# Kernel tuning notes

Hardware: AMD Instinct MI355X
Metric: run time of the kernel (lower is better)

Reference implementation:

```python
import jax, jax.numpy as jnp
import numpy as np

WH, WW = 7, 7
N = WH * WW
NUM_HEADS = 12
DIM = 384
NUM_WINDOWS = 64
B = 64

def _relative_position_index(wh, ww):
    ch, cw = np.meshgrid(np.arange(wh), np.arange(ww), indexing='ij')
    coords = np.stack([ch, cw]).reshape(2, -1)            # [2, N]
    rel = coords[:, :, None] - coords[:, None, :]         # [2, N, N]
    rel = rel.transpose(1, 2, 0).astype(np.int64)         # [N, N, 2]
    rel[:, :, 0] += wh - 1
    rel[:, :, 1] += ww - 1
    rel[:, :, 0] *= 2 * ww - 1
    return rel.sum(-1)                                    # [N, N]

REL_IDX = jnp.asarray(_relative_position_index(WH, WW))  # [N, N] int

def setup_inputs() -> dict:
    key = jax.random.key(0)
    ks = jax.random.split(key, 4)
    s = 0.02
    return {
        'x': jax.random.normal(ks[0], (NUM_WINDOWS * B, N, DIM), jnp.float32),
        'mask': jnp.zeros((NUM_WINDOWS, N, N), jnp.float32),
        'w_qkv': jax.random.normal(ks[1], (3 * DIM, DIM), jnp.float32) * s,
        'b_qkv': jnp.zeros((3 * DIM,), jnp.float32),
        'w_proj': jax.random.normal(ks[2], (DIM, DIM), jnp.float32) * s,
        'b_proj': jnp.zeros((DIM,), jnp.float32),
        'bias_table': jax.random.normal(ks[3], (169, NUM_HEADS), jnp.float32) * s,
    }

def reference(x, mask, w_qkv, b_qkv, w_proj, b_proj, bias_table):
    bn, n, dim = x.shape
    h = NUM_HEADS
    d = dim // h
    scale = d ** -0.5
    # qkv projection: [bn, n, 3*dim] -> q,k,v each [bn, h, n, d]
    qkv = x @ w_qkv.T + b_qkv
    qkv = qkv.reshape(bn, n, 3, h, d).transpose(2, 0, 3, 1, 4)
    q, k, v = qkv[0], qkv[1], qkv[2]
    # windowed QK^T
    scores = jnp.einsum('bhid,bhjd->bhij', q, k) * scale
    # gathered relative position bias: [N, N, h] -> [h, N, N]
    rel_bias = bias_table[REL_IDX]                       # [N, N, h]
    scores = scores + rel_bias.transpose(2, 0, 1)[None]  # [bn, h, N, N]
    # additive window mask; batch layout is (num_windows, B)
    num_w = mask.shape[0]
    scores = scores.reshape(num_w, bn // num_w, h, n, n) + mask[:, None, None, :, :]
    scores = scores.reshape(bn, h, n, n)
    probs = jax.nn.softmax(scores, axis=-1)
    ctx = jnp.einsum('bhij,bhjd->bhid', probs, v)
    ctx = ctx.transpose(0, 2, 1, 3).reshape(bn, n, dim)  # b i (h d)
    return ctx @ w_proj.T + b_proj
```

## Files before the change

### kernel.cpp

```cpp
#include <hip/hip_runtime.h>
#include <hip/hip_fp16.h>

#define NTOK   49
#define DIMM   384
#define NHEAD  12
#define HD     32
#define BNWIN  4096

typedef _Float16 half8 __attribute__((ext_vector_type(8)));
typedef float    f32x4 __attribute__((ext_vector_type(4)));

#define WQF_OFF   0u
#define WPF_OFF   884736u
#define RBM_OFF   1179648u
#define XHF_OFF   8555520u

__global__ __launch_bounds__(256) void prep_kernel(
    const float* __restrict__ wqkv, const float* __restrict__ wproj,
    const float* __restrict__ btab, const float* __restrict__ mask,
    _Float16* __restrict__ wqf, _Float16* __restrict__ wpf,
    float* __restrict__ rbm)
{
    int idx = blockIdx.x * 256 + threadIdx.x;
    if (idx < 55296) {
        int lane = idx & 63;
        int kk   = (idx >> 6) % 12;
        int T    = idx / 768;
        const float* s = wqkv + (size_t)(T * 16 + (lane & 15)) * DIMM + kk * 32 + (lane >> 4) * 8;
        _Float16* d = wqf + (size_t)idx * 8;
#pragma unroll
        for (int e = 0; e < 8; ++e) d[e] = (_Float16)s[e];
    }
    if (idx < 18432) {
        int lane = idx & 63;
        int kk   = (idx >> 6) % 12;
        int T    = idx / 768;
        const float* s = wproj + (size_t)(T * 16 + (lane & 15)) * DIMM + kk * 32 + (lane >> 4) * 8;
        _Float16* d = wpf + (size_t)idx * 8;
#pragma unroll
        for (int e = 0; e < 8; ++e) d[e] = (_Float16)s[e];
    }
    if (idx < 1843968) {
        int wm  = idx / 28812;
        int rem = idx - wm * 28812;
        int h   = rem / 2401;
        int ij  = rem - h * 2401;
        int i   = ij / 49;
        int j   = ij - i * 49;
        int ih = i / 7, iw = i - ih * 7;
        int jh = j / 7, jw = j - jh * 7;
        int rel = (ih - jh + 6) * 13 + (iw - jw + 6);
        rbm[idx] = btab[rel * 12 + h] + mask[wm * 2401 + ij];
    }
}

__global__ __launch_bounds__(256) void xswz_kernel(
    const float* __restrict__ x, _Float16* __restrict__ xh)
{
    const int total = BNWIN * 12 * NTOK * 4;
    int g = blockIdx.x * 256 + threadIdx.x;
    const int step = gridDim.x * 256;
    for (; g < total; g += step) {
        int quad = g & 3;
        int t    = g >> 2;
        int row  = t % 49;
        int t2   = t / 49;
        int k    = t2 % 12;
        int bn   = t2 / 12;
        const float* s = x + ((size_t)bn * NTOK + row) * DIMM + k * 32 + quad * 8;
        float4 a0 = *(const float4*)s;
        float4 a1 = *(const float4*)(s + 4);
        half8 v;
        v[0] = (_Float16)a0.x; v[1] = (_Float16)a0.y;
        v[2] = (_Float16)a0.z; v[3] = (_Float16)a0.w;
        v[4] = (_Float16)a1.x; v[5] = (_Float16)a1.y;
        v[6] = (_Float16)a1.z; v[7] = (_Float16)a1.w;
        *(half8*)(xh + (size_t)g * 8) = v;
    }
}

__global__ __launch_bounds__(256, 3) void attn_kernel(
    const _Float16* __restrict__ xh,
    const _Float16* __restrict__ wq, const float* __restrict__ bq,
    const float* __restrict__ rbm,
    const _Float16* __restrict__ wp, const float* __restrict__ bp,
    float* __restrict__ out)
{
    __shared__ _Float16 smem[4][6224];
    const int tid  = threadIdx.x;
    const int wv   = tid >> 6;
    const int lane = tid & 63;
    const int quad = lane >> 4;
    const int l16  = lane & 15;
    const int bn   = blockIdx.x;
    const int wm   = bn >> 6;

    _Float16* q_s  = &smem[wv][0];
    _Float16* k_s  = &smem[wv][1960];
    _Float16* p_s  = &smem[wv][0];
    _Float16* vT_s = &smem[wv][3920];
    _Float16* cl   = &smem[0][0];

    const float scale = 0.17677669529663687f;

    int rowm[4];
#pragma unroll
    for (int mi = 0; mi < 4; ++mi) {
        int r = mi * 16 + l16;
        rowm[mi] = r > 48 ? 48 : r;
    }

    auto load_af = [&](int k, half8* af) {
        const _Float16* base = xh + ((size_t)(bn * 12 + k) * NTOK) * 32 + quad * 8;
#pragma unroll
        for (int mi = 0; mi < 4; ++mi)
            af[mi] = *(const half8*)(base + rowm[mi] * 32);
    };
    auto load_bf = [&](const _Float16* w, int T, int k) -> half8 {
        return *(const half8*)(w + ((size_t)(T * 12 + k) * 64 + lane) * 8);
    };

    half8 oh[2][4];
    f32x4 o2[4][2];

    for (int hh = 0; hh < 3; ++hh) {
        const int h = wv + (hh << 2);

        {
            f32x4 av[2][4];
#pragma unroll
            for (int nv = 0; nv < 2; ++nv)
#pragma unroll
                for (int mi = 0; mi < 4; ++mi)
                    av[nv][mi] = (f32x4){0.f, 0.f, 0.f, 0.f};

#pragma unroll 4
            for (int k = 0; k < 12; ++k) {
                half8 af[4];
                load_af(k, af);
#pragma unroll
                for (int nv = 0; nv < 2; ++nv) {
                    const int T = 48 + h * 2 + nv;
                    half8 bf = load_bf(wq, T, k);
#pragma unroll
                    for (int mi = 0; mi < 4; ++mi)
                        av[nv][mi] = __builtin_amdgcn_mfma_f32_16x16x32_f16(af[mi], bf, av[nv][mi], 0, 0, 0);
                }
            }
#pragma unroll
            for (int nv = 0; nv < 2; ++nv) {
                const float bias = bq[(48 + h * 2 + nv) * 16 + l16];
                const int colh = nv * 16 + l16;
#pragma unroll
                for (int mi = 0; mi < 4; ++mi)
#pragma unroll
                    for (int r = 0; r < 4; ++r) {
                        const int row = mi * 16 + quad * 4 + r;
                        vT_s[colh * 72 + row] = (_Float16)(av[nv][mi][r] + bias);
                    }
            }
        }

        {
            f32x4 aqk[4][4];
#pragma unroll
            for (int nn = 0; nn < 4; ++nn)
#pragma unroll
                for (int mi = 0; mi < 4; ++mi)
                    aqk[nn][mi] = (f32x4){0.f, 0.f, 0.f, 0.f};

#pragma unroll 2
            for (int k = 0; k < 12; ++k) {
                half8 af[4];
                load_af(k, af);
#pragma unroll
                for (int nn = 0; nn < 4; ++nn) {
                    const int T = (nn < 2) ? (h * 2 + nn) : (24 + h * 2 + (nn - 2));
                    half8 bf = load_bf(wq, T, k);
#pragma unroll
                    for (int mi = 0; mi < 4; ++mi)
                        aqk[nn][mi] = __builtin_amdgcn_mfma_f32_16x16x32_f16(af[mi], bf, aqk[nn][mi], 0, 0, 0);
                }
            }
#pragma unroll
            for (int nn = 0; nn < 4; ++nn) {
                const int T = (nn < 2) ? (h * 2 + nn) : (24 + h * 2 + (nn - 2));
                const float bias = bq[T * 16 + l16];
                const int colh = (nn & 1) * 16 + l16;
                if (nn < 2) {
                    const float bs = bias * scale;
#pragma unroll
                    for (int mi = 0; mi < 4; ++mi)
#pragma unroll
                        for (int r = 0; r < 4; ++r) {
                            const int row = mi * 16 + quad * 4 + r;
                            if (row < 49) q_s[row * 40 + colh] = (_Float16)(aqk[nn][mi][r] * scale + bs);
                        }
                } else {
#pragma unroll
                    for (int mi = 0; mi < 4; ++mi)
#pragma unroll
                        for (int r = 0; r < 4; ++r) {
                            const int row = mi * 16 + quad * 4 + r;
                            if (row < 49) k_s[row * 40 + colh] = (_Float16)(aqk[nn][mi][r] + bias);
                        }
                }
            }
        }

        f32x4 s[4][4];
        {
            half8 bk[4];
#pragma unroll
            for (int nj = 0; nj < 4; ++nj)
                bk[nj] = *(const half8*)(k_s + rowm[nj] * 40 + quad * 8);
#pragma unroll
            for (int mi = 0; mi < 4; ++mi) {
                half8 aq = *(const half8*)(q_s + rowm[mi] * 40 + quad * 8);
#pragma unroll
                for (int nj = 0; nj < 4; ++nj)
                    s[mi][nj] = __builtin_amdgcn_mfma_f32_16x16x32_f16(
                        aq, bk[nj], (f32x4){0.f, 0.f, 0.f, 0.f}, 0, 0, 0);
            }
        }

        const float* rbmh = rbm + (size_t)(wm * 12 + h) * 2401;
#pragma unroll
        for (int mi = 0; mi < 4; ++mi) {
#pragma unroll
            for (int r = 0; r < 4; ++r) {
                const int i  = mi * 16 + quad * 4 + r;
                const int iq = i > 48 ? 48 : i;
                float vals[4];
                float mx = -3.0e38f;
#pragma unroll
                for (int nj = 0; nj < 4; ++nj) {
                    const int j = nj * 16 + l16;
                    float v = -1.0e30f;
                    if (j < 49)
                        v = s[mi][nj][r] + rbmh[iq * 49 + j];
                    vals[nj] = v;
                    mx = fmaxf(mx, v);
                }
#pragma unroll
                for (int off = 8; off >= 1; off >>= 1)
                    mx = fmaxf(mx, __shfl_xor(mx, off));
                float sum = 0.f;
#pragma unroll
                for (int nj = 0; nj < 4; ++nj) {
                    vals[nj] = __expf(vals[nj] - mx);
                    sum += vals[nj];
                }
#pragma unroll
                for (int off = 8; off >= 1; off >>= 1)
                    sum += __shfl_xor(sum, off);
                const float inv = __builtin_amdgcn_rcpf(sum);
                if (i < 49) {
#pragma unroll
                    for (int nj = 0; nj < 4; ++nj)
                        p_s[i * 72 + nj * 16 + l16] = (_Float16)(vals[nj] * inv);
                }
            }
        }

        f32x4 o[4][2];
#pragma unroll
        for (int mi = 0; mi < 4; ++mi)
#pragma unroll
            for (int nd = 0; nd < 2; ++nd)
                o[mi][nd] = (f32x4){0.f, 0.f, 0.f, 0.f};
#pragma unroll
        for (int ks = 0; ks < 2; ++ks) {
            half8 bv[2];
#pragma unroll
            for (int nd = 0; nd < 2; ++nd)
                bv[nd] = *(const half8*)(vT_s + (nd * 16 + l16) * 72 + ks * 32 + quad * 8);
#pragma unroll
            for (int mi = 0; mi < 4; ++mi) {
                half8 apf = *(const half8*)(p_s + rowm[mi] * 72 + ks * 32 + quad * 8);
#pragma unroll
                for (int nd = 0; nd < 2; ++nd)
                    o[mi][nd] = __builtin_amdgcn_mfma_f32_16x16x32_f16(apf, bv[nd], o[mi][nd], 0, 0, 0);
            }
        }

        if (hh < 2) {
#pragma unroll
            for (int mi = 0; mi < 4; ++mi) {
                half8 t;
#pragma unroll
                for (int nd = 0; nd < 2; ++nd)
#pragma unroll
                    for (int r = 0; r < 4; ++r)
                        t[nd * 4 + r] = (_Float16)o[mi][nd][r];
                oh[hh][mi] = t;
            }
        } else {
#pragma unroll
            for (int mi = 0; mi < 4; ++mi)
#pragma unroll
                for (int nd = 0; nd < 2; ++nd)
                    o2[mi][nd] = o[mi][nd];
        }
    }

    __syncthreads();
#pragma unroll
    for (int hh = 0; hh < 2; ++hh) {
        const int h = wv + (hh << 2);
#pragma unroll
        for (int mi = 0; mi < 4; ++mi)
#pragma unroll
            for (int nd = 0; nd < 2; ++nd)
#pragma unroll
                for (int r = 0; r < 4; ++r) {
                    const int row = mi * 16 + quad * 4 + r;
                    if (row < 49)
                        cl[row * 400 + h * HD + nd * 16 + l16] = oh[hh][mi][nd * 4 + r];
                }
    }
    {
        const int h = wv + 8;
#pragma unroll
        for (int mi = 0; mi < 4; ++mi)
#pragma unroll
            for (int nd = 0; nd < 2; ++nd)
#pragma unroll
                for (int r = 0; r < 4; ++r) {
                    const int row = mi * 16 + quad * 4 + r;
                    if (row < 49)
                        cl[row * 400 + h * HD + nd * 16 + l16] = (_Float16)o2[mi][nd][r];
                }
    }
    __syncthreads();

    {
        f32x4 c[6][4];
#pragma unroll
        for (int nj = 0; nj < 6; ++nj)
#pragma unroll
            for (int mi = 0; mi < 4; ++mi)
                c[nj][mi] = (f32x4){0.f, 0.f, 0.f, 0.f};

#pragma unroll 2
        for (int k = 0; k < 12; ++k) {
            half8 a[4];
#pragma unroll
            for (int mi = 0; mi < 4; ++mi)
                a[mi] = *(const half8*)(cl + rowm[mi] * 400 + k * 32 + quad * 8);
#pragma unroll
            for (int nj = 0; nj < 6; ++nj) {
                half8 b = load_bf(wp, wv * 6 + nj, k);
#pragma unroll
                for (int mi = 0; mi < 4; ++mi)
                    c[nj][mi] = __builtin_amdgcn_mfma_f32_16x16x32_f16(a[mi], b, c[nj][mi], 0, 0, 0);
            }
        }
#pragma unroll
        for (int nj = 0; nj < 6; ++nj) {
            const int n = (wv * 6 + nj) * 16 + l16;
            const float bias = bp[n];
#pragma unroll
            for (int mi = 0; mi < 4; ++mi) {
#pragma unroll
                for (int r = 0; r < 4; ++r) {
                    const int i = mi * 16 + quad * 4 + r;
                    if (i < 49)
                        out[((size_t)bn * NTOK + i) * DIMM + n] = c[nj][mi][r] + bias;
                }
            }
        }
    }
}

extern "C" void kernel_launch(void* const* d_in, const int* in_sizes, int n_in,
                              void* d_out, int out_size, void* d_ws, size_t ws_size,
                              hipStream_t stream)
{
    const float* x     = (const float*)d_in[0];
    const float* mask  = (const float*)d_in[1];
    const float* wqkv  = (const float*)d_in[2];
    const float* bqkv  = (const float*)d_in[3];
    const float* wproj = (const float*)d_in[4];
    const float* bproj = (const float*)d_in[5];
    const float* btab  = (const float*)d_in[6];
    float* out = (float*)d_out;

    char* ws = (char*)d_ws;
    _Float16* wq_f = (_Float16*)(ws + WQF_OFF);
    _Float16* wp_f = (_Float16*)(ws + WPF_OFF);
    float*    rbm  = (float*)(ws + RBM_OFF);
    _Float16* xh_f = (_Float16*)(ws + XHF_OFF);

    hipLaunchKernelGGL(prep_kernel, dim3(7203), dim3(256), 0, stream,
                       wqkv, wproj, btab, mask, wq_f, wp_f, rbm);
    hipLaunchKernelGGL(xswz_kernel, dim3(2048), dim3(256), 0, stream, x, xh_f);
    hipLaunchKernelGGL(attn_kernel, dim3(BNWIN), dim3(256), 0, stream,
                       xh_f, wq_f, bqkv, rbm, wp_f, bproj, out);
}
```

Measured before the change: 1.543 ms.

## Fuse QKV projections, pre-swizzle fp16 bias-mask, stage output stores through LDS

Q, K and V projections are merged into a single k-loop with six accumulator tiles, so each x fragment is loaded once per head instead of twice. The relative-bias-plus-mask table is precomputed in fp16, laid out to match the MFMA fragment layout, and padded with a large negative value, so each lane does vector loads without bounds checks. Blocks are remapped so consecutive blocks hit different mask windows. The output tile is staged through LDS for coalesced float4 global stores, and the LDS row stride is padded to cut bank conflicts. The costs are higher register pressure from 24 accumulators and extra barriers around the two store passes.

Result: faster. 1.440 ms (-6.7%).

```diff
diff --git a/kernel.cpp b/kernel.cpp
--- a/kernel.cpp
+++ b/kernel.cpp
@@ -8,18 +8,19 @@
 #define BNWIN  4096
 
 typedef _Float16 half8 __attribute__((ext_vector_type(8)));
+typedef _Float16 half4 __attribute__((ext_vector_type(4)));
 typedef float    f32x4 __attribute__((ext_vector_type(4)));
 
 #define WQF_OFF   0u
 #define WPF_OFF   884736u
-#define RBM_OFF   1179648u
-#define XHF_OFF   8555520u
+#define RBMF_OFF  1179648u
+#define XHF_OFF   7471104u
 
 __global__ __launch_bounds__(256) void prep_kernel(
     const float* __restrict__ wqkv, const float* __restrict__ wproj,
     const float* __restrict__ btab, const float* __restrict__ mask,
     _Float16* __restrict__ wqf, _Float16* __restrict__ wpf,
-    float* __restrict__ rbm)
+    _Float16* __restrict__ rbmf)
 {
     int idx = blockIdx.x * 256 + threadIdx.x;
     if (idx < 55296) {
@@ -40,17 +41,28 @@
 #pragma unroll
         for (int e = 0; e < 8; ++e) d[e] = (_Float16)s[e];
     }
-    if (idx < 1843968) {
-        int wm  = idx / 28812;
-        int rem = idx - wm * 28812;
-        int h   = rem / 2401;
-        int ij  = rem - h * 2401;
-        int i   = ij / 49;
-        int j   = ij - i * 49;
-        int ih = i / 7, iw = i - ih * 7;
-        int jh = j / 7, jw = j - jh * 7;
-        int rel = (ih - jh + 6) * 13 + (iw - jw + 6);
-        rbm[idx] = btab[rel * 12 + h] + mask[wm * 2401 + ij];
+    if (idx < 3145728) {
+        int wm  = idx >> 15;
+        wm = idx / 49152;
+        int rem = idx - wm * 49152;
+        int h   = rem / 4096;
+        int e   = rem - h * 4096;
+        int r    = e & 3;
+        int lane = (e >> 2) & 63;
+        int t    = e >> 8;
+        int nj   = t & 3;
+        int mi   = t >> 2;
+        int i = mi * 16 + (lane >> 4) * 4 + r;
+        int j = nj * 16 + (lane & 15);
+        float val = -30000.f;
+        if (j < 49) {
+            int ii = i > 48 ? 48 : i;
+            int ih = ii / 7, iw = ii - ih * 7;
+            int jh = j / 7,  jw = j - jh * 7;
+            int rel = (ih - jh + 6) * 13 + (iw - jw + 6);
+            val = btab[rel * 12 + h] + mask[wm * 2401 + ii * 49 + j];
+        }
+        rbmf[idx] = (_Float16)val;
     }
 }
 
@@ -82,7 +94,7 @@
 __global__ __launch_bounds__(256, 3) void attn_kernel(
     const _Float16* __restrict__ xh,
     const _Float16* __restrict__ wq, const float* __restrict__ bq,
-    const float* __restrict__ rbm,
+    const _Float16* __restrict__ rbmf,
     const _Float16* __restrict__ wp, const float* __restrict__ bp,
     float* __restrict__ out)
 {
@@ -92,7 +104,7 @@
     const int lane = tid & 63;
     const int quad = lane >> 4;
     const int l16  = lane & 15;
-    const int bn   = blockIdx.x;
+    const int bn   = ((blockIdx.x & 7) << 9) | (blockIdx.x >> 3);
     const int wm   = bn >> 6;
 
     _Float16* q_s  = &smem[wv][0];
@@ -100,6 +112,7 @@
     _Float16* p_s  = &smem[wv][0];
     _Float16* vT_s = &smem[wv][3920];
     _Float16* cl   = &smem[0][0];
+    float*    fls  = (float*)&smem[0][0];
 
     const float scale = 0.17677669529663687f;
 
@@ -125,86 +138,60 @@
 
     for (int hh = 0; hh < 3; ++hh) {
         const int h = wv + (hh << 2);
-
-        {
-            f32x4 av[2][4];
-#pragma unroll
-            for (int nv = 0; nv < 2; ++nv)
+        int tT[6];
+        tT[0] = h * 2;      tT[1] = h * 2 + 1;
+        tT[2] = 24 + h * 2; tT[3] = 25 + h * 2;
+        tT[4] = 48 + h * 2; tT[5] = 49 + h * 2;
+
+        f32x4 acc[6][4];
+#pragma unroll
+        for (int t = 0; t < 6; ++t)
+#pragma unroll
+            for (int mi = 0; mi < 4; ++mi)
+                acc[t][mi] = (f32x4){0.f, 0.f, 0.f, 0.f};
+
+#pragma unroll 2
+        for (int k = 0; k < 12; ++k) {
+            half8 af[4];
+            load_af(k, af);
+#pragma unroll
+            for (int t = 0; t < 6; ++t) {
+                half8 bf = load_bf(wq, tT[t], k);
 #pragma unroll
                 for (int mi = 0; mi < 4; ++mi)
-                    av[nv][mi] = (f32x4){0.f, 0.f, 0.f, 0.f};
-
-#pragma unroll 4
-            for (int k = 0; k < 12; ++k) {
-                half8 af[4];
-                load_af(k, af);
-#pragma unroll
-                for (int nv = 0; nv < 2; ++nv) {
-                    const int T = 48 + h * 2 + nv;
-                    half8 bf = load_bf(wq, T, k);
-#pragma unroll
-                    for (int mi = 0; mi < 4; ++mi)
-                        av[nv][mi] = __builtin_amdgcn_mfma_f32_16x16x32_f16(af[mi], bf, av[nv][mi], 0, 0, 0);
-                }
-            }
-#pragma unroll
-            for (int nv = 0; nv < 2; ++nv) {
-                const float bias = bq[(48 + h * 2 + nv) * 16 + l16];
-                const int colh = nv * 16 + l16;
+                    acc[t][mi] = __builtin_amdgcn_mfma_f32_16x16x32_f16(af[mi], bf, acc[t][mi], 0, 0, 0);
+            }
+        }
+
+#pragma unroll
+        for (int t = 0; t < 6; ++t) {
+            const float bias = bq[tT[t] * 16 + l16];
+            const int colh = (t & 1) * 16 + l16;
+            if (t < 2) {
+                const float bs = bias * scale;
 #pragma unroll
                 for (int mi = 0; mi < 4; ++mi)
 #pragma unroll
                     for (int r = 0; r < 4; ++r) {
                         const int row = mi * 16 + quad * 4 + r;
-                        vT_s[colh * 72 + row] = (_Float16)(av[nv][mi][r] + bias);
+                        if (row < 49) q_s[row * 40 + colh] = (_Float16)(acc[t][mi][r] * scale + bs);
                     }
-            }
-        }
-
-        {
-            f32x4 aqk[4][4];
-#pragma unroll
-            for (int nn = 0; nn < 4; ++nn)
+            } else if (t < 4) {
 #pragma unroll
                 for (int mi = 0; mi < 4; ++mi)
-                    aqk[nn][mi] = (f32x4){0.f, 0.f, 0.f, 0.f};
-
-#pragma unroll 2
-            for (int k = 0; k < 12; ++k) {
-                half8 af[4];
-                load_af(k, af);
-#pragma unroll
-                for (int nn = 0; nn < 4; ++nn) {
-                    const int T = (nn < 2) ? (h * 2 + nn) : (24 + h * 2 + (nn - 2));
-                    half8 bf = load_bf(wq, T, k);
-#pragma unroll
-                    for (int mi = 0; mi < 4; ++mi)
-                        aqk[nn][mi] = __builtin_amdgcn_mfma_f32_16x16x32_f16(af[mi], bf, aqk[nn][mi], 0, 0, 0);
-                }
-            }
-#pragma unroll
-            for (int nn = 0; nn < 4; ++nn) {
-                const int T = (nn < 2) ? (h * 2 + nn) : (24 + h * 2 + (nn - 2));
-                const float bias = bq[T * 16 + l16];
-                const int colh = (nn & 1) * 16 + l16;
-                if (nn < 2) {
-                    const float bs = bias * scale;
-#pragma unroll
-                    for (int mi = 0; mi < 4; ++mi)
-#pragma unroll
-                        for (int r = 0; r < 4; ++r) {
-                            const int row = mi * 16 + quad * 4 + r;
-                            if (row < 49) q_s[row * 40 + colh] = (_Float16)(aqk[nn][mi][r] * scale + bs);
-                        }
-                } else {
-#pragma unroll
-                    for (int mi = 0; mi < 4; ++mi)
-#pragma unroll
-                        for (int r = 0; r < 4; ++r) {
-                            const int row = mi * 16 + quad * 4 + r;
-                            if (row < 49) k_s[row * 40 + colh] = (_Float16)(aqk[nn][mi][r] + bias);
-                        }
-                }
+#pragma unroll
+                    for (int r = 0; r < 4; ++r) {
+                        const int row = mi * 16 + quad * 4 + r;
+                        if (row < 49) k_s[row * 40 + colh] = (_Float16)(acc[t][mi][r] + bias);
+                    }
+            } else {
+#pragma unroll
+                for (int mi = 0; mi < 4; ++mi)
+#pragma unroll
+                    for (int r = 0; r < 4; ++r) {
+                        const int row = mi * 16 + quad * 4 + r;
+                        vT_s[colh * 72 + row] = (_Float16)(acc[t][mi][r] + bias);
+                    }
             }
         }
 
@@ -224,21 +211,21 @@
             }
         }
 
-        const float* rbmh = rbm + (size_t)(wm * 12 + h) * 2401;
+        const _Float16* rbmh = rbmf + (size_t)(wm * 12 + h) * 4096;
 #pragma unroll
         for (int mi = 0; mi < 4; ++mi) {
+            half4 rv[4];
+#pragma unroll
+            for (int nj = 0; nj < 4; ++nj)
+                rv[nj] = *(const half4*)(rbmh + ((mi * 4 + nj) * 64 + lane) * 4);
 #pragma unroll
             for (int r = 0; r < 4; ++r) {
-                const int i  = mi * 16 + quad * 4 + r;
-                const int iq = i > 48 ? 48 : i;
+                const int i = mi * 16 + quad * 4 + r;
                 float vals[4];
                 float mx = -3.0e38f;
 #pragma unroll
                 for (int nj = 0; nj < 4; ++nj) {
-                    const int j = nj * 16 + l16;
-                    float v = -1.0e30f;
-                    if (j < 49)
-                        v = s[mi][nj][r] + rbmh[iq * 49 + j];
+                    float v = s[mi][nj][r] + (float)rv[nj][r];
                     vals[nj] = v;
                     mx = fmaxf(mx, v);
                 }
@@ -316,7 +303,7 @@
                 for (int r = 0; r < 4; ++r) {
                     const int row = mi * 16 + quad * 4 + r;
                     if (row < 49)
-                        cl[row * 400 + h * HD + nd * 16 + l16] = oh[hh][mi][nd * 4 + r];
+                        cl[row * 404 + h * HD + nd * 16 + l16] = oh[hh][mi][nd * 4 + r];
                 }
     }
     {
@@ -329,46 +316,60 @@
                 for (int r = 0; r < 4; ++r) {
                     const int row = mi * 16 + quad * 4 + r;
                     if (row < 49)
-                        cl[row * 400 + h * HD + nd * 16 + l16] = (_Float16)o2[mi][nd][r];
+                        cl[row * 404 + h * HD + nd * 16 + l16] = (_Float16)o2[mi][nd][r];
                 }
     }
     __syncthreads();
 
-    {
-        f32x4 c[6][4];
-#pragma unroll
-        for (int nj = 0; nj < 6; ++nj)
+    f32x4 c[6][4];
+#pragma unroll
+    for (int nj = 0; nj < 6; ++nj)
+#pragma unroll
+        for (int mi = 0; mi < 4; ++mi)
+            c[nj][mi] = (f32x4){0.f, 0.f, 0.f, 0.f};
+
+#pragma unroll 2
+    for (int k = 0; k < 12; ++k) {
+        half8 a[4];
+#pragma unroll
+        for (int mi = 0; mi < 4; ++mi)
+            a[mi] = *(const half8*)(cl + rowm[mi] * 404 + k * 32 + quad * 8);
+#pragma unroll
+        for (int nj = 0; nj < 6; ++nj) {
+            half8 b = load_bf(wp, wv * 6 + nj, k);
 #pragma unroll
             for (int mi = 0; mi < 4; ++mi)
-                c[nj][mi] = (f32x4){0.f, 0.f, 0.f, 0.f};
-
-#pragma unroll 2
-        for (int k = 0; k < 12; ++k) {
-            half8 a[4];
-#pragma unroll
-            for (int mi = 0; mi < 4; ++mi)
-                a[mi] = *(const half8*)(cl + rowm[mi] * 400 + k * 32 + quad * 8);
-#pragma unroll
-            for (int nj = 0; nj < 6; ++nj) {
-                half8 b = load_bf(wp, wv * 6 + nj, k);
+                c[nj][mi] = __builtin_amdgcn_mfma_f32_16x16x32_f16(a[mi], b, c[nj][mi], 0, 0, 0);
+        }
+    }
+
+    float bias6[6];
+#pragma unroll
+    for (int nj = 0; nj < 6; ++nj)
+        bias6[nj] = bp[wv * 96 + nj * 16 + l16];
+
+#pragma unroll 1
+    for (int pass = 0; pass < 2; ++pass) {
+        __syncthreads();
+        if ((wv >> 1) == pass) {
+            const int cbase = (wv & 1) * 96;
+#pragma unroll
+            for (int nj = 0; nj < 6; ++nj)
 #pragma unroll
                 for (int mi = 0; mi < 4; ++mi)
-                    c[nj][mi] = __builtin_amdgcn_mfma_f32_16x16x32_f16(a[mi], b, c[nj][mi], 0, 0, 0);
-            }
-        }
-#pragma unroll
-        for (int nj = 0; nj < 6; ++nj) {
-            const int n = (wv * 6 + nj) * 16 + l16;
-            const float bias = bp[n];
-#pragma unroll
-            for (int mi = 0; mi < 4; ++mi) {
-#pragma unroll
-                for (int r = 0; r < 4; ++r) {
-                    const int i = mi * 16 + quad * 4 + r;
-                    if (i < 49)
-                        out[((size_t)bn * NTOK + i) * DIMM + n] = c[nj][mi][r] + bias;
-                }
-            }
+#pragma unroll
+                    for (int r = 0; r < 4; ++r) {
+                        const int row = mi * 16 + quad * 4 + r;
+                        if (row < 49)
+                            fls[row * 196 + cbase + nj * 16 + l16] = c[nj][mi][r] + bias6[nj];
+                    }
+        }
+        __syncthreads();
+        for (int g = tid; g < 2352; g += 256) {
+            const int row = g / 48;
+            const int c4  = g - row * 48;
+            float4 v = *(const float4*)(fls + row * 196 + c4 * 4);
+            *(float4*)(out + ((size_t)bn * NTOK + row) * DIMM + pass * 192 + c4 * 4) = v;
         }
     }
 }
@@ -387,14 +388,14 @@
     float* out = (float*)d_out;
 
     char* ws = (char*)d_ws;
-    _Float16* wq_f = (_Float16*)(ws + WQF_OFF);
-    _Float16* wp_f = (_Float16*)(ws + WPF_OFF);
-    float*    rbm  = (float*)(ws + RBM_OFF);
-    _Float16* xh_f = (_Float16*)(ws + XHF_OFF);
-
-    hipLaunchKernelGGL(prep_kernel, dim3(7203), dim3(256), 0, stream,
-                       wqkv, wproj, btab, mask, wq_f, wp_f, rbm);
+    _Float16* wq_f  = (_Float16*)(ws + WQF_OFF);
+    _Float16* wp_f  = (_Float16*)(ws + WPF_OFF);
+    _Float16* rbm_f = (_Float16*)(ws + RBMF_OFF);
+    _Float16* xh_f  = (_Float16*)(ws + XHF_OFF);
+
+    hipLaunchKernelGGL(prep_kernel, dim3(12288), dim3(256), 0, stream,
+                       wqkv, wproj, btab, mask, wq_f, wp_f, rbm_f);
     hipLaunchKernelGGL(xswz_kernel, dim3(2048), dim3(256), 0, stream, x, xh_f);
     hipLaunchKernelGGL(attn_kernel, dim3(BNWIN), dim3(256), 0, stream,
-                       xh_f, wq_f, bqkv, rbm, wp_f, bproj, out);
+                       xh_f, wq_f, bqkv, rbm_f, wp_f, bproj, out);
 }
```
